# Kernel optimization log

Measured on AMD Instinct MI355X. Metric: run time of the kernel, lower is better.

## Reference

```python
import jax, jax.numpy as jnp
import numpy as np

N = 100000
IN_C = 256
OUT_C = 128
NHEAD = 4
NUM_CLASSES = 1000


def setup_inputs() -> dict:
    key = jax.random.key(0)
    ks = jax.random.split(key, 6)
    context_h = jax.random.normal(ks[0], (N, IN_C), dtype=jnp.float32)
    W_lin = jax.random.normal(ks[1], (NHEAD * OUT_C, IN_C), dtype=jnp.float32) * 0.05
    b_lin = jax.random.normal(ks[2], (NHEAD * OUT_C,), dtype=jnp.float32) * 0.05
    W_att = jax.random.normal(ks[3], (OUT_C,), dtype=jnp.float32) * 0.05
    b_att = jax.random.normal(ks[4], (1,), dtype=jnp.float32) * 0.05
    context_y = jax.random.randint(ks[5], (N,), 0, NUM_CLASSES, dtype=jnp.int32)
    return {
        "context_h": context_h,
        "W_lin": W_lin,
        "b_lin": b_lin,
        "W_att": W_att,
        "b_att": b_att,
        "context_y": context_y,
        "num_classes": NUM_CLASSES,
    }


def reference(context_h, W_lin, b_lin, W_att, b_att, context_y, num_classes):
    # Linear projection: [N, nhead*out_c] -> [N, nhead, out_c]
    h = context_h @ W_lin.T + b_lin
    n = context_h.shape[0]
    ht = h.reshape(n, NHEAD, OUT_C)
    # per-head attention score: [N, nhead]
    score = jnp.einsum("nho,o->nh", ht, W_att) + b_att[0]
    score = jnp.where(score >= 0, score, 0.2 * score)  # leaky_relu(0.2)
    # scatter softmax over segments context_y (stable two-pass)
    seg_max = jax.ops.segment_max(score, context_y, num_segments=num_classes)
    p = jnp.exp(score - seg_max[context_y])  # [N, nhead]
    denom = jax.ops.segment_sum(p, context_y, num_segments=num_classes)
    att_w = p / denom[context_y]  # [N, nhead]
    # weighted scatter-add pooling: [N, nhead, in_c] -> [C, nhead, in_c]
    att_h = context_h[:, None, :] * att_w[:, :, None]
    pooled = jax.ops.segment_sum(att_h, context_y, num_segments=num_classes)
    return pooled.reshape(num_classes, NHEAD * IN_C)
```

## Files before the change

### kernel.cpp

```cpp
#include <hip/hip_runtime.h>
#include <math.h>

#define N_ROWS 100000
#define IN_C   256
#define OUT_C  128
#define NHEAD  4
#define NCLS   1000
#define NCOPY  16
#define CAP    64

#define OFF_V      0
#define OFF_CB     1024
#define OFF_CNT    1032
#define OFF_BUCKET 17032

__global__ __launch_bounds__(256) void k_prep(const float* __restrict__ W_lin,
                                              const float* __restrict__ b_lin,
                                              const float* __restrict__ W_att,
                                              const float* __restrict__ b_att,
                                              float* __restrict__ ws) {
    const int b = blockIdx.x, t = threadIdx.x;
    if (b >= NHEAD) {
        int i = (b - NHEAD) * 256 + t;
        if (i < NCOPY * NCLS) ((unsigned*)(ws + OFF_CNT))[i] = 0u;
        return;
    }
    __shared__ float sw[OUT_C];
    __shared__ float rb[256];
    if (t < OUT_C) sw[t] = W_att[t];
    __syncthreads();
    const float* wl = W_lin + (size_t)(b * OUT_C) * IN_C + t;
    float s0 = 0.f, s1 = 0.f, s2 = 0.f, s3 = 0.f;
    #pragma unroll 8
    for (int o = 0; o < OUT_C; o += 4) {
        s0 = fmaf(wl[(size_t)(o + 0) * IN_C], sw[o + 0], s0);
        s1 = fmaf(wl[(size_t)(o + 1) * IN_C], sw[o + 1], s1);
        s2 = fmaf(wl[(size_t)(o + 2) * IN_C], sw[o + 2], s2);
        s3 = fmaf(wl[(size_t)(o + 3) * IN_C], sw[o + 3], s3);
    }
    (ws + OFF_V)[b * IN_C + t] = (s0 + s1) + (s2 + s3);
    rb[t] = (t < OUT_C) ? b_lin[b * OUT_C + t] * sw[t] : 0.f;
    __syncthreads();
    for (int d = 128; d; d >>= 1) {
        if (t < d) rb[t] += rb[t + d];
        __syncthreads();
    }
    if (t == 0) (ws + OFF_CB)[b] = rb[0] + b_att[0];
}

__global__ __launch_bounds__(256) void k_bucket(const int* __restrict__ y,
                                                float* __restrict__ ws) {
    int n0 = (blockIdx.x * 256 + threadIdx.x) * 2;
    if (n0 >= N_ROWS) return;
    unsigned* cnt    = (unsigned*)(ws + OFF_CNT);
    unsigned* bucket = (unsigned*)(ws + OFF_BUCKET);
    int2 yv = *(const int2*)(y + n0);
    unsigned cp = (blockIdx.x & (NCOPY - 1)) * NCLS;
    unsigned i0 = cp + (unsigned)yv.x;
    unsigned p0 = atomicAdd(&cnt[i0], 1u);
    if (p0 < CAP) bucket[i0 * CAP + p0] = (unsigned)n0;
    unsigned i1 = cp + (unsigned)yv.y;
    unsigned p1 = atomicAdd(&cnt[i1], 1u);
    if (p1 < CAP) bucket[i1 * CAP + p1] = (unsigned)(n0 + 1);
}

__global__ __launch_bounds__(512) void k_pool(const float* __restrict__ ch,
                                              float* __restrict__ out,
                                              const float* __restrict__ ws) {
    __shared__ unsigned rowbuf[NCOPY * CAP];
    __shared__ float4   sAcc[NHEAD][4][64];
    __shared__ float4   sDs[8];
    const int c = blockIdx.x, t = threadIdx.x;
    const int wave = t >> 6, lane = t & 63;
    const unsigned* cntA   = (const unsigned*)(ws + OFF_CNT);
    const unsigned* bucket = (const unsigned*)(ws + OFF_BUCKET);
    float* o = out + (size_t)c * (NHEAD * IN_C);

    unsigned cc[NCOPY], pre[NCOPY];
    unsigned cnt = 0;
    #pragma unroll
    for (int cp = 0; cp < NCOPY; ++cp) {
        unsigned v = cntA[cp * NCLS + c];
        cc[cp] = v > CAP ? CAP : v;
        pre[cp] = cnt;
        cnt += cc[cp];
    }
    if (cnt == 0) {
        if (t < 256) ((float4*)o)[t] = make_float4(0.f, 0.f, 0.f, 0.f);
        return;
    }
    for (int tt = t; tt < NCOPY * CAP; tt += 512) {
        int cp = tt >> 6, j = tt & (CAP - 1);
        if ((unsigned)j < cc[cp])
            rowbuf[pre[cp] + j] = bucket[(cp * NCLS + c) * CAP + j];
    }
    __syncthreads();

    const float4* V4 = (const float4*)(ws + OFF_V);
    float4 v0 = V4[0 * 64 + lane];
    float4 v1 = V4[1 * 64 + lane];
    float4 v2 = V4[2 * 64 + lane];
    float4 v3 = V4[3 * 64 + lane];
    float4 cbv = *(const float4*)(ws + OFF_CB);
    float cb = (lane & 1) ? ((lane & 2) ? cbv.w : cbv.y)
                          : ((lane & 2) ? cbv.z : cbv.x);

    const float4* ch4 = (const float4*)ch;
    const float4 z = make_float4(0.f, 0.f, 0.f, 0.f);

    float4 a0 = z, a1 = z, a2 = z, a3 = z, dsum = z;
    {
        unsigned r = 2 * (unsigned)wave;
        float4 xA0 = z, xA1 = z, xB0 = z, xB1 = z, xC0 = z, xC1 = z;
        if (r < cnt)      xA0 = ch4[(size_t)rowbuf[r] * 64 + lane];
        if (r + 1 < cnt)  xA1 = ch4[(size_t)rowbuf[r + 1] * 64 + lane];
        if (r + 16 < cnt) xB0 = ch4[(size_t)rowbuf[r + 16] * 64 + lane];
        if (r + 17 < cnt) xB1 = ch4[(size_t)rowbuf[r + 17] * 64 + lane];
        if (r + 32 < cnt) xC0 = ch4[(size_t)rowbuf[r + 32] * 64 + lane];
        if (r + 33 < cnt) xC1 = ch4[(size_t)rowbuf[r + 33] * 64 + lane];
        for (; r < cnt; r += 16) {
            unsigned rd = r + 48;
            float4 xD0 = z, xD1 = z;
            if (rd < cnt)     xD0 = ch4[(size_t)rowbuf[rd] * 64 + lane];
            if (rd + 1 < cnt) xD1 = ch4[(size_t)rowbuf[rd + 1] * 64 + lane];

            #pragma unroll
            for (int k = 0; k < 2; ++k) {
                const float4 x = k ? xA1 : xA0;
                const float g = k ? ((r + 1 < cnt) ? 1.f : 0.f) : 1.f;
                float p0 = x.x * v0.x + x.y * v0.y + x.z * v0.z + x.w * v0.w;
                float p1 = x.x * v1.x + x.y * v1.y + x.z * v1.z + x.w * v1.w;
                float p2 = x.x * v2.x + x.y * v2.y + x.z * v2.z + x.w * v2.w;
                float p3 = x.x * v3.x + x.y * v3.y + x.z * v3.z + x.w * v3.w;
                float a01 = (lane & 1) ? p1 : p0;
                float b01 = (lane & 1) ? p0 : p1;
                b01 = __shfl_xor(b01, 1);  a01 += b01;
                float a23 = (lane & 1) ? p3 : p2;
                float b23 = (lane & 1) ? p2 : p3;
                b23 = __shfl_xor(b23, 1);  a23 += b23;
                float e = (lane & 2) ? a23 : a01;
                float f = (lane & 2) ? a01 : a23;
                f = __shfl_xor(f, 2);      e += f;
                e += __shfl_xor(e, 4);
                e += __shfl_xor(e, 8);
                e += __shfl_xor(e, 16);
                e += __shfl_xor(e, 32);
                float s = e + cb;
                s = s >= 0.0f ? s : 0.2f * s;
                float pe = __expf(s) * g;
                float h0 = __shfl(pe, 0), h1 = __shfl(pe, 1);
                float h2 = __shfl(pe, 2), h3 = __shfl(pe, 3);
                dsum.x += h0; dsum.y += h1; dsum.z += h2; dsum.w += h3;
                a0.x = fmaf(x.x, h0, a0.x); a0.y = fmaf(x.y, h0, a0.y);
                a0.z = fmaf(x.z, h0, a0.z); a0.w = fmaf(x.w, h0, a0.w);
                a1.x = fmaf(x.x, h1, a1.x); a1.y = fmaf(x.y, h1, a1.y);
                a1.z = fmaf(x.z, h1, a1.z); a1.w = fmaf(x.w, h1, a1.w);
                a2.x = fmaf(x.x, h2, a2.x); a2.y = fmaf(x.y, h2, a2.y);
                a2.z = fmaf(x.z, h2, a2.z); a2.w = fmaf(x.w, h2, a2.w);
                a3.x = fmaf(x.x, h3, a3.x); a3.y = fmaf(x.y, h3, a3.y);
                a3.z = fmaf(x.z, h3, a3.z); a3.w = fmaf(x.w, h3, a3.w);
            }
            xA0 = xB0; xA1 = xB1; xB0 = xC0; xB1 = xC1; xC0 = xD0; xC1 = xD1;
        }
    }
    if (wave < 4) {
        sAcc[0][wave][lane] = a0; sAcc[1][wave][lane] = a1;
        sAcc[2][wave][lane] = a2; sAcc[3][wave][lane] = a3;
    }
    if (lane == 0) sDs[wave] = dsum;
    __syncthreads();
    if (wave >= 4) {
        int w = wave - 4;
        float4 q;
        q = sAcc[0][w][lane]; q.x += a0.x; q.y += a0.y; q.z += a0.z; q.w += a0.w; sAcc[0][w][lane] = q;
        q = sAcc[1][w][lane]; q.x += a1.x; q.y += a1.y; q.z += a1.z; q.w += a1.w; sAcc[1][w][lane] = q;
        q = sAcc[2][w][lane]; q.x += a2.x; q.y += a2.y; q.z += a2.z; q.w += a2.w; sAcc[2][w][lane] = q;
        q = sAcc[3][w][lane]; q.x += a3.x; q.y += a3.y; q.z += a3.z; q.w += a3.w; sAcc[3][w][lane] = q;
    }
    __syncthreads();

    if (wave < NHEAD) {
        float4 q0 = sAcc[wave][0][lane], q1 = sAcc[wave][1][lane],
               q2 = sAcc[wave][2][lane], q3 = sAcc[wave][3][lane];
        float4 acc = make_float4((q0.x + q1.x) + (q2.x + q3.x),
                                 (q0.y + q1.y) + (q2.y + q3.y),
                                 (q0.z + q1.z) + (q2.z + q3.z),
                                 (q0.w + q1.w) + (q2.w + q3.w));
        float4 d0 = sDs[0], d1 = sDs[1], d2 = sDs[2], d3 = sDs[3];
        float4 d4 = sDs[4], d5 = sDs[5], d6 = sDs[6], d7 = sDs[7];
        float4 dt = make_float4(((d0.x + d1.x) + (d2.x + d3.x)) + ((d4.x + d5.x) + (d6.x + d7.x)),
                                ((d0.y + d1.y) + (d2.y + d3.y)) + ((d4.y + d5.y) + (d6.y + d7.y)),
                                ((d0.z + d1.z) + (d2.z + d3.z)) + ((d4.z + d5.z) + (d6.z + d7.z)),
                                ((d0.w + d1.w) + (d2.w + d3.w)) + ((d4.w + d5.w) + (d6.w + d7.w)));
        float dh = (wave == 0) ? dt.x : (wave == 1) ? dt.y : (wave == 2) ? dt.z : dt.w;
        float inv = 1.0f / dh;
        ((float4*)o)[wave * 64 + lane] =
            make_float4(acc.x * inv, acc.y * inv, acc.z * inv, acc.w * inv);
    }
}

extern "C" void kernel_launch(void* const* d_in, const int* in_sizes, int n_in,
                              void* d_out, int out_size, void* d_ws, size_t ws_size,
                              hipStream_t stream) {
    const float* ch    = (const float*)d_in[0];
    const float* W_lin = (const float*)d_in[1];
    const float* b_lin = (const float*)d_in[2];
    const float* W_att = (const float*)d_in[3];
    const float* b_att = (const float*)d_in[4];
    const int*   y     = (const int*)d_in[5];
    float* out = (float*)d_out;
    float* ws  = (float*)d_ws;

    k_prep  <<<NHEAD + 63, 256, 0, stream>>>(W_lin, b_lin, W_att, b_att, ws);
    k_bucket<<<(N_ROWS / 2 + 255) / 256, 256, 0, stream>>>(y, ws);
    k_pool  <<<NCLS, 512, 0, stream>>>(ch, out, ws);
}
```

Measured before the change: 185.0 us.

## Batch eight rows per wave with interleaved shuffle reductions and vector index loads

The pool kernel now gives each wave eight consecutive rows per iteration instead of two rows spread across a three-stage prefetch ring. It reads row indices from shared memory as uint4 and interleaves the eight independent shuffle-reduction chains to expose more instruction-level parallelism. The weight and bias loads are moved ahead of the bucket gather so their latency overlaps the barrier. The cost is a shallower prefetch (one batch ahead) and higher register pressure from sixteen live float4 rows, which may reduce occupancy.

New measurement: 195.2 us. 5.5% more time.

```diff
diff --git a/kernel.cpp b/kernel.cpp
--- a/kernel.cpp
+++ b/kernel.cpp
@@ -67,7 +67,7 @@
 __global__ __launch_bounds__(512) void k_pool(const float* __restrict__ ch,
                                               float* __restrict__ out,
                                               const float* __restrict__ ws) {
-    __shared__ unsigned rowbuf[NCOPY * CAP];
+    __shared__ unsigned rowbuf[NCOPY * CAP + 8];
     __shared__ float4   sAcc[NHEAD][4][64];
     __shared__ float4   sDs[8];
     const int c = blockIdx.x, t = threadIdx.x;
@@ -89,12 +89,6 @@
         if (t < 256) ((float4*)o)[t] = make_float4(0.f, 0.f, 0.f, 0.f);
         return;
     }
-    for (int tt = t; tt < NCOPY * CAP; tt += 512) {
-        int cp = tt >> 6, j = tt & (CAP - 1);
-        if ((unsigned)j < cc[cp])
-            rowbuf[pre[cp] + j] = bucket[(cp * NCLS + c) * CAP + j];
-    }
-    __syncthreads();
 
     const float4* V4 = (const float4*)(ws + OFF_V);
     float4 v0 = V4[0 * 64 + lane];
@@ -105,64 +99,119 @@
     float cb = (lane & 1) ? ((lane & 2) ? cbv.w : cbv.y)
                           : ((lane & 2) ? cbv.z : cbv.x);
 
+    for (int tt = t; tt < NCOPY * CAP; tt += 512) {
+        int cp = tt >> 6, j = tt & (CAP - 1);
+        if ((unsigned)j < cc[cp])
+            rowbuf[pre[cp] + j] = bucket[(cp * NCLS + c) * CAP + j];
+    }
+    __syncthreads();
+
     const float4* ch4 = (const float4*)ch;
+    const uint4*  rb4 = (const uint4*)rowbuf;
     const float4 z = make_float4(0.f, 0.f, 0.f, 0.f);
 
     float4 a0 = z, a1 = z, a2 = z, a3 = z, dsum = z;
+
     {
-        unsigned r = 2 * (unsigned)wave;
-        float4 xA0 = z, xA1 = z, xB0 = z, xB1 = z, xC0 = z, xC1 = z;
-        if (r < cnt)      xA0 = ch4[(size_t)rowbuf[r] * 64 + lane];
-        if (r + 1 < cnt)  xA1 = ch4[(size_t)rowbuf[r + 1] * 64 + lane];
-        if (r + 16 < cnt) xB0 = ch4[(size_t)rowbuf[r + 16] * 64 + lane];
-        if (r + 17 < cnt) xB1 = ch4[(size_t)rowbuf[r + 17] * 64 + lane];
-        if (r + 32 < cnt) xC0 = ch4[(size_t)rowbuf[r + 32] * 64 + lane];
-        if (r + 33 < cnt) xC1 = ch4[(size_t)rowbuf[r + 33] * 64 + lane];
-        for (; r < cnt; r += 16) {
-            unsigned rd = r + 48;
-            float4 xD0 = z, xD1 = z;
-            if (rd < cnt)     xD0 = ch4[(size_t)rowbuf[rd] * 64 + lane];
-            if (rd + 1 < cnt) xD1 = ch4[(size_t)rowbuf[rd + 1] * 64 + lane];
-
-            #pragma unroll
-            for (int k = 0; k < 2; ++k) {
-                const float4 x = k ? xA1 : xA0;
-                const float g = k ? ((r + 1 < cnt) ? 1.f : 0.f) : 1.f;
-                float p0 = x.x * v0.x + x.y * v0.y + x.z * v0.z + x.w * v0.w;
-                float p1 = x.x * v1.x + x.y * v1.y + x.z * v1.z + x.w * v1.w;
-                float p2 = x.x * v2.x + x.y * v2.y + x.z * v2.z + x.w * v2.w;
-                float p3 = x.x * v3.x + x.y * v3.y + x.z * v3.z + x.w * v3.w;
-                float a01 = (lane & 1) ? p1 : p0;
-                float b01 = (lane & 1) ? p0 : p1;
-                b01 = __shfl_xor(b01, 1);  a01 += b01;
-                float a23 = (lane & 1) ? p3 : p2;
-                float b23 = (lane & 1) ? p2 : p3;
-                b23 = __shfl_xor(b23, 1);  a23 += b23;
-                float e = (lane & 2) ? a23 : a01;
-                float f = (lane & 2) ? a01 : a23;
-                f = __shfl_xor(f, 2);      e += f;
-                e += __shfl_xor(e, 4);
-                e += __shfl_xor(e, 8);
-                e += __shfl_xor(e, 16);
-                e += __shfl_xor(e, 32);
-                float s = e + cb;
-                s = s >= 0.0f ? s : 0.2f * s;
-                float pe = __expf(s) * g;
-                float h0 = __shfl(pe, 0), h1 = __shfl(pe, 1);
-                float h2 = __shfl(pe, 2), h3 = __shfl(pe, 3);
-                dsum.x += h0; dsum.y += h1; dsum.z += h2; dsum.w += h3;
-                a0.x = fmaf(x.x, h0, a0.x); a0.y = fmaf(x.y, h0, a0.y);
-                a0.z = fmaf(x.z, h0, a0.z); a0.w = fmaf(x.w, h0, a0.w);
-                a1.x = fmaf(x.x, h1, a1.x); a1.y = fmaf(x.y, h1, a1.y);
-                a1.z = fmaf(x.z, h1, a1.z); a1.w = fmaf(x.w, h1, a1.w);
-                a2.x = fmaf(x.x, h2, a2.x); a2.y = fmaf(x.y, h2, a2.y);
-                a2.z = fmaf(x.z, h2, a2.z); a2.w = fmaf(x.w, h2, a2.w);
-                a3.x = fmaf(x.x, h3, a3.x); a3.y = fmaf(x.y, h3, a3.y);
-                a3.z = fmaf(x.z, h3, a3.z); a3.w = fmaf(x.w, h3, a3.w);
+        unsigned r = 8u * (unsigned)wave;
+        float4 xA0 = z, xA1 = z, xA2 = z, xA3 = z,
+               xA4 = z, xA5 = z, xA6 = z, xA7 = z;
+        if (r < cnt) {
+            uint4 iL = rb4[r >> 2], iH = rb4[(r >> 2) + 1];
+                 xA0 = ch4[(size_t)iL.x * 64 + lane];
+            if (r + 1 < cnt)  xA1 = ch4[(size_t)iL.y * 64 + lane];
+            if (r + 2 < cnt)  xA2 = ch4[(size_t)iL.z * 64 + lane];
+            if (r + 3 < cnt)  xA3 = ch4[(size_t)iL.w * 64 + lane];
+            if (r + 4 < cnt)  xA4 = ch4[(size_t)iH.x * 64 + lane];
+            if (r + 5 < cnt)  xA5 = ch4[(size_t)iH.y * 64 + lane];
+            if (r + 6 < cnt)  xA6 = ch4[(size_t)iH.z * 64 + lane];
+            if (r + 7 < cnt)  xA7 = ch4[(size_t)iH.w * 64 + lane];
+        }
+        for (; r < cnt; r += 64) {
+            unsigned rn = r + 64;
+            float4 xB0 = z, xB1 = z, xB2 = z, xB3 = z,
+                   xB4 = z, xB5 = z, xB6 = z, xB7 = z;
+            if (rn < cnt) {
+                uint4 jL = rb4[rn >> 2], jH = rb4[(rn >> 2) + 1];
+                       xB0 = ch4[(size_t)jL.x * 64 + lane];
+                if (rn + 1 < cnt)  xB1 = ch4[(size_t)jL.y * 64 + lane];
+                if (rn + 2 < cnt)  xB2 = ch4[(size_t)jL.z * 64 + lane];
+                if (rn + 3 < cnt)  xB3 = ch4[(size_t)jL.w * 64 + lane];
+                if (rn + 4 < cnt)  xB4 = ch4[(size_t)jH.x * 64 + lane];
+                if (rn + 5 < cnt)  xB5 = ch4[(size_t)jH.y * 64 + lane];
+                if (rn + 6 < cnt)  xB6 = ch4[(size_t)jH.z * 64 + lane];
+                if (rn + 7 < cnt)  xB7 = ch4[(size_t)jH.w * 64 + lane];
             }
-            xA0 = xB0; xA1 = xB1; xB0 = xC0; xB1 = xC1; xC0 = xD0; xC1 = xD1;
+
+            float e0, e1, e2, e3, e4, e5, e6, e7;
+#define QSCORE(X_, E_) do {                                                    \
+            float p0 = X_.x * v0.x + X_.y * v0.y + X_.z * v0.z + X_.w * v0.w;  \
+            float p1 = X_.x * v1.x + X_.y * v1.y + X_.z * v1.z + X_.w * v1.w;  \
+            float p2 = X_.x * v2.x + X_.y * v2.y + X_.z * v2.z + X_.w * v2.w;  \
+            float p3 = X_.x * v3.x + X_.y * v3.y + X_.z * v3.z + X_.w * v3.w;  \
+            float a01 = (lane & 1) ? p1 : p0;                                  \
+            float b01 = (lane & 1) ? p0 : p1;                                  \
+            b01 = __shfl_xor(b01, 1);  a01 += b01;                             \
+            float a23 = (lane & 1) ? p3 : p2;                                  \
+            float b23 = (lane & 1) ? p2 : p3;                                  \
+            b23 = __shfl_xor(b23, 1);  a23 += b23;                             \
+            E_ = (lane & 2) ? a23 : a01;                                       \
+            float f2 = (lane & 2) ? a01 : a23;                                 \
+            f2 = __shfl_xor(f2, 2);    E_ += f2;                               \
+        } while (0)
+            QSCORE(xA0, e0); QSCORE(xA1, e1); QSCORE(xA2, e2); QSCORE(xA3, e3);
+            QSCORE(xA4, e4); QSCORE(xA5, e5); QSCORE(xA6, e6); QSCORE(xA7, e7);
+#undef QSCORE
+
+            e0 += __shfl_xor(e0, 4);  e1 += __shfl_xor(e1, 4);
+            e2 += __shfl_xor(e2, 4);  e3 += __shfl_xor(e3, 4);
+            e4 += __shfl_xor(e4, 4);  e5 += __shfl_xor(e5, 4);
+            e6 += __shfl_xor(e6, 4);  e7 += __shfl_xor(e7, 4);
+            e0 += __shfl_xor(e0, 8);  e1 += __shfl_xor(e1, 8);
+            e2 += __shfl_xor(e2, 8);  e3 += __shfl_xor(e3, 8);
+            e4 += __shfl_xor(e4, 8);  e5 += __shfl_xor(e5, 8);
+            e6 += __shfl_xor(e6, 8);  e7 += __shfl_xor(e7, 8);
+            e0 += __shfl_xor(e0, 16); e1 += __shfl_xor(e1, 16);
+            e2 += __shfl_xor(e2, 16); e3 += __shfl_xor(e3, 16);
+            e4 += __shfl_xor(e4, 16); e5 += __shfl_xor(e5, 16);
+            e6 += __shfl_xor(e6, 16); e7 += __shfl_xor(e7, 16);
+            e0 += __shfl_xor(e0, 32); e1 += __shfl_xor(e1, 32);
+            e2 += __shfl_xor(e2, 32); e3 += __shfl_xor(e3, 32);
+            e4 += __shfl_xor(e4, 32); e5 += __shfl_xor(e5, 32);
+            e6 += __shfl_xor(e6, 32); e7 += __shfl_xor(e7, 32);
+
+            float pe0, pe1, pe2, pe3, pe4, pe5, pe6, pe7;
+#define PEXP(E_, J_, P_) do {                                                  \
+            float s = E_ + cb;                                                 \
+            s = s >= 0.0f ? s : 0.2f * s;                                      \
+            P_ = __expf(s) * ((r + (unsigned)(J_) < cnt) ? 1.f : 0.f);         \
+        } while (0)
+            PEXP(e0, 0, pe0); PEXP(e1, 1, pe1); PEXP(e2, 2, pe2); PEXP(e3, 3, pe3);
+            PEXP(e4, 4, pe4); PEXP(e5, 5, pe5); PEXP(e6, 6, pe6); PEXP(e7, 7, pe7);
+#undef PEXP
+
+#define ACC(X_, P_) do {                                                       \
+            float h0 = __shfl(P_, 0), h1 = __shfl(P_, 1);                      \
+            float h2 = __shfl(P_, 2), h3 = __shfl(P_, 3);                      \
+            dsum.x += h0; dsum.y += h1; dsum.z += h2; dsum.w += h3;            \
+            a0.x = fmaf(X_.x, h0, a0.x); a0.y = fmaf(X_.y, h0, a0.y);          \
+            a0.z = fmaf(X_.z, h0, a0.z); a0.w = fmaf(X_.w, h0, a0.w);          \
+            a1.x = fmaf(X_.x, h1, a1.x); a1.y = fmaf(X_.y, h1, a1.y);          \
+            a1.z = fmaf(X_.z, h1, a1.z); a1.w = fmaf(X_.w, h1, a1.w);          \
+            a2.x = fmaf(X_.x, h2, a2.x); a2.y = fmaf(X_.y, h2, a2.y);          \
+            a2.z = fmaf(X_.z, h2, a2.z); a2.w = fmaf(X_.w, h2, a2.w);          \
+            a3.x = fmaf(X_.x, h3, a3.x); a3.y = fmaf(X_.y, h3, a3.y);          \
+            a3.z = fmaf(X_.z, h3, a3.z); a3.w = fmaf(X_.w, h3, a3.w);          \
+        } while (0)
+            ACC(xA0, pe0); ACC(xA1, pe1); ACC(xA2, pe2); ACC(xA3, pe3);
+            ACC(xA4, pe4); ACC(xA5, pe5); ACC(xA6, pe6); ACC(xA7, pe7);
+#undef ACC
+
+            xA0 = xB0; xA1 = xB1; xA2 = xB2; xA3 = xB3;
+            xA4 = xB4; xA5 = xB5; xA6 = xB6; xA7 = xB7;
         }
     }
+
     if (wave < 4) {
         sAcc[0][wave][lane] = a0; sAcc[1][wave][lane] = a1;
         sAcc[2][wave][lane] = a2; sAcc[3][wave][lane] = a3;
```
